# Kernel tuning notes

Measured on AMD Instinct MI355X. Metric: run time of the kernel, lower is better.

Reference implementation:

```python
import jax, jax.numpy as jnp
import numpy as np

N_NODES = 100000
HIDDEN = 128
N_CLASSES = 8


def _sage_conv(x, src, dst, Wl, bl, Wr, num_nodes):
    # PyG SAGEConv (aggr='mean'): out = lin_l(mean_{j in N(i)} x_j) + lin_r(x_i)
    agg = jax.ops.segment_sum(x[src], dst, num_segments=num_nodes)          # [N, H]
    deg = jax.ops.segment_sum(jnp.ones((src.shape[0],), x.dtype), dst,
                              num_segments=num_nodes)                       # [N]
    mean = agg / jnp.maximum(deg, 1.0)[:, None]
    return mean @ Wl + bl + x @ Wr


def setup_inputs() -> dict:
    key = jax.random.key(0)
    ks = jax.random.split(key, 12)
    s = 1.0 / np.sqrt(HIDDEN)
    inp = {
        "node_emb": jax.random.normal(ks[0], (N_NODES, HIDDEN), jnp.float32),
        "Wl0": jax.random.normal(ks[1], (HIDDEN, HIDDEN), jnp.float32) * s,
        "bl0": jnp.zeros((HIDDEN,), jnp.float32),
        "Wr0": jax.random.normal(ks[2], (HIDDEN, HIDDEN), jnp.float32) * s,
        "Wl1": jax.random.normal(ks[3], (HIDDEN, HIDDEN), jnp.float32) * s,
        "bl1": jnp.zeros((HIDDEN,), jnp.float32),
        "Wr1": jax.random.normal(ks[4], (HIDDEN, HIDDEN), jnp.float32) * s,
        "mlp_W1": jax.random.normal(ks[5], (2 * HIDDEN, HIDDEN), jnp.float32) * (1.0 / np.sqrt(2 * HIDDEN)),
        "mlp_b1": jnp.zeros((HIDDEN,), jnp.float32),
        "mlp_W2": jax.random.normal(ks[6], (HIDDEN, N_CLASSES), jnp.float32) * s,
        "mlp_b2": jnp.zeros((N_CLASSES,), jnp.float32),
        "edge_index": jax.random.randint(ks[7], (2, 1600000), 0, N_NODES, jnp.int64),
        "edge_q": jax.random.randint(ks[8], (2, 500000), 0, N_NODES, jnp.int64),
    }
    return inp


def reference(node_emb, Wl0, bl0, Wr0, Wl1, bl1, Wr1,
              mlp_W1, mlp_b1, mlp_W2, mlp_b2, edge_index, edge_q):
    src, dst = edge_index[0], edge_index[1]
    n = node_emb.shape[0]
    # layer 0 + relu (dropout is identity in eval / p=0)
    x = jax.nn.relu(_sage_conv(node_emb, src, dst, Wl0, bl0, Wr0, n))
    # layer 1 + relu
    x = jax.nn.relu(_sage_conv(x, src, dst, Wl1, bl1, Wr1, n))
    # edge classifier: gather endpoint pairs, concat, 2-layer MLP
    qs, qd = edge_q[0], edge_q[1]
    edge_feat = jnp.concatenate([x[qs], x[qd]], axis=-1)   # [Eq, 2H]
    h = jax.nn.relu(edge_feat @ mlp_W1 + mlp_b1)
    logits = h @ mlp_W2 + mlp_b2                            # [Eq, C]
    return logits
```

## Files before the change

kernel.cpp:

```cpp
#include <hip/hip_runtime.h>
#include <hip/hip_bf16.h>
#include <cstdint>
#include <cstddef>

#define HID 128
#define SH 9
#define NODES_PER_BIN 512

typedef __attribute__((ext_vector_type(8))) __bf16 bf16x8;
typedef __attribute__((ext_vector_type(4))) float floatx4;

__device__ __forceinline__ ushort f2bf(float f) {
    uint u = __float_as_uint(f);
    u += 0x7fff + ((u >> 16) & 1);
    return (ushort)(u >> 16);
}
__device__ __forceinline__ float bf2f(uint h) { return __uint_as_float(h << 16); }

__device__ __forceinline__ void async16(const ushort* g, ushort* l) {
    __builtin_amdgcn_global_load_lds(
        (const __attribute__((address_space(1))) uint*)g,
        (__attribute__((address_space(3))) uint*)l, 16, 0, 0);
}


__global__ void k_hist(const int* __restrict__ dst, int E, int* __restrict__ binc) {
    __shared__ int h[256];
    int t = threadIdx.x;
    h[t] = 0;
    __syncthreads();
    for (int e = blockIdx.x * 256 + t; e < E; e += gridDim.x * 256)
        atomicAdd(&h[dst[e] >> SH], 1);
    __syncthreads();
    if (h[t]) atomicAdd(&binc[t], h[t]);
}

__global__ void k_binscan(const int* __restrict__ binc, int* __restrict__ bin_start,
                          int* __restrict__ bin_cursor, int E) {
    __shared__ int s[256];
    int t = threadIdx.x;
    int c = binc[t];
    s[t] = c;
    __syncthreads();
    #pragma unroll
    for (int off = 1; off < 256; off <<= 1) {
        int add = (t >= off) ? s[t - off] : 0;
        __syncthreads();
        s[t] += add;
        __syncthreads();
    }
    int excl = s[t] - c;
    bin_start[t] = excl;
    bin_cursor[t] = excl;
    if (t == 255) bin_start[256] = E;
}

__global__ __launch_bounds__(256) void k_part(
    const int* __restrict__ src, const int* __restrict__ dst, int E,
    int* __restrict__ bin_cursor, uint* __restrict__ ebuf) {
    __shared__ int h[256];
    __shared__ int sc[256];
    __shared__ int rk[256];
    __shared__ int gb[256];
    __shared__ uint2 ro[2048];
    int t = threadIdx.x;
    int base = blockIdx.x * 2048;
    h[t] = 0;
    __syncthreads();
    int dd[8], ss[8];
    bool ok[8];
    #pragma unroll
    for (int k = 0; k < 8; ++k) {
        int e = base + k * 256 + t;
        ok[k] = e < E;
        if (ok[k]) {
            dd[k] = dst[e];
            ss[k] = src[e];
            atomicAdd(&h[dd[k] >> SH], 1);
        }
    }
    __syncthreads();
    sc[t] = h[t];
    __syncthreads();
    #pragma unroll
    for (int off = 1; off < 256; off <<= 1) {
        int add = (t >= off) ? sc[t - off] : 0;
        __syncthreads();
        sc[t] += add;
        __syncthreads();
    }
    rk[t] = sc[t] - h[t];
    {
        int c = h[t];
        if (c > 0) gb[t] = atomicAdd(&bin_cursor[t], c);
    }
    __syncthreads();
    #pragma unroll
    for (int k = 0; k < 8; ++k) {
        if (ok[k]) {
            int bin = dd[k] >> SH;
            int r = atomicAdd(&rk[bin], 1);
            ro[r] = make_uint2((uint)dd[k],
                               ((uint)(dd[k] & (NODES_PER_BIN - 1)) << 23) | (uint)ss[k]);
        }
    }
    __syncthreads();
    int nv = sc[255];
    for (int i = t; i < nv; i += 256) {
        uint2 pr = ro[i];
        int bin = (int)(pr.x >> SH);
        int excl = sc[bin] - h[bin];
        ebuf[gb[bin] + (i - excl)] = pr.y;
    }
}

__global__ __launch_bounds__(256) void k_csr(
    const uint* __restrict__ ebuf, const int* __restrict__ bin_start,
    int* __restrict__ rowptr, int* __restrict__ csr, int N, int E, int NB) {
    __shared__ int cnt[512];
    __shared__ int p[256];
    __shared__ int excl[512];
    int t = threadIdx.x;
    int b = blockIdx.x;
    int d0 = b << SH;
    int ebase = bin_start[b], eend = bin_start[b + 1];
    cnt[t] = 0; cnt[t + 256] = 0;
    __syncthreads();
    for (int e = ebase + t; e < eend; e += 256)
        atomicAdd(&cnt[ebuf[e] >> 23], 1);
    __syncthreads();
    p[t] = cnt[2 * t] + cnt[2 * t + 1];
    __syncthreads();
    #pragma unroll
    for (int off = 1; off < 256; off <<= 1) {
        int add = (t >= off) ? p[t - off] : 0;
        __syncthreads();
        p[t] += add;
        __syncthreads();
    }
    int e0 = (t == 0) ? 0 : p[t - 1];
    excl[2 * t] = e0;
    excl[2 * t + 1] = e0 + cnt[2 * t];
    __syncthreads();
    #pragma unroll
    for (int i = t; i < 512; i += 256) {
        int node = d0 + i;
        if (node < N) rowptr[node] = ebase + excl[i];
    }
    if (b == NB - 1 && t == 0) rowptr[N] = E;
    __syncthreads();
    for (int e = ebase + t; e < eend; e += 256) {
        uint w = ebuf[e];
        int r = atomicAdd(&excl[w >> 23], 1);
        csr[ebase + r] = (int)(w & 0x7FFFFFu);
    }
}


__global__ void k_cvt(const float* __restrict__ in, ushort* __restrict__ out, int n4) {
    int i = blockIdx.x * blockDim.x + threadIdx.x;
    if (i < n4) {
        float4 v = ((const float4*)in)[i];
        ushort4 o;
        o.x = f2bf(v.x); o.y = f2bf(v.y); o.z = f2bf(v.z); o.w = f2bf(v.w);
        ((ushort4*)out)[i] = o;
    }
}

__global__ void k_prepw(const float* __restrict__ Wl0, const float* __restrict__ Wr0,
                        const float* __restrict__ Wl1, const float* __restrict__ Wr1,
                        const float* __restrict__ W1,  const float* __restrict__ W2,
                        ushort* __restrict__ WlrT0, ushort* __restrict__ WlrT1,
                        ushort* __restrict__ W1T,   ushort* __restrict__ W2T) {
    int idx = blockIdx.x * 256 + threadIdx.x;
    if (idx < 32768) {
        int n = idx >> 8, k = idx & 255;
        float v = (k < 128) ? Wl0[k * 128 + n] : Wr0[(k - 128) * 128 + n];
        WlrT0[n * 256 + k] = f2bf(v);
    } else if (idx < 65536) {
        int t = idx - 32768; int n = t >> 8, k = t & 255;
        float v = (k < 128) ? Wl1[k * 128 + n] : Wr1[(k - 128) * 128 + n];
        WlrT1[n * 256 + k] = f2bf(v);
    } else if (idx < 98304) {
        int t = idx - 65536; int n = t >> 8, k = t & 255;
        W1T[n * 256 + k] = f2bf(W1[k * 128 + n]);
    } else if (idx < 100352) {
        int t = idx - 98304; int n = t >> 7, k = t & 127;
        W2T[n * 128 + k] = (n < 8) ? f2bf(W2[k * 8 + n]) : (ushort)0;
    }
}

__global__ __launch_bounds__(256) void k_agg16(const ushort* __restrict__ x,
                                               const int* __restrict__ rowptr,
                                               const int* __restrict__ csr,
                                               ushort* __restrict__ mean, int N) {
    int node = blockIdx.x * 4 + (threadIdx.x >> 6);
    if (node >= N) return;
    int l = threadIdx.x & 63;
    int lh = l & 31, hi = l >> 5;
    int b = rowptr[node], e = rowptr[node + 1];
    const uint2* xv = (const uint2*)x;
    float a0 = 0.f, a1 = 0.f, a2 = 0.f, a3 = 0.f;
    for (int j = b; j < e; j += 4) {
        int r0 = j + hi, r1 = j + 2 + hi;
        if (r0 < e) {
            uint2 v = xv[(size_t)csr[r0] * 32 + lh];
            a0 += bf2f(v.x & 0xffffu); a1 += bf2f(v.x >> 16);
            a2 += bf2f(v.y & 0xffffu); a3 += bf2f(v.y >> 16);
        }
        if (r1 < e) {
            uint2 v = xv[(size_t)csr[r1] * 32 + lh];
            a0 += bf2f(v.x & 0xffffu); a1 += bf2f(v.x >> 16);
            a2 += bf2f(v.y & 0xffffu); a3 += bf2f(v.y >> 16);
        }
    }
    a0 += __shfl_xor(a0, 32);
    a1 += __shfl_xor(a1, 32);
    a2 += __shfl_xor(a2, 32);
    a3 += __shfl_xor(a3, 32);
    if (hi == 0) {
        float inv = 1.f / fmaxf((float)(e - b), 1.f);
        uint2 o;
        o.x = (uint)f2bf(a0 * inv) | ((uint)f2bf(a1 * inv) << 16);
        o.y = (uint)f2bf(a2 * inv) | ((uint)f2bf(a3 * inv) << 16);
        ((uint2*)mean)[(size_t)node * 32 + lh] = o;
    }
}

__global__ __launch_bounds__(256) void k_gemm16(
    const ushort* __restrict__ Alo, const ushort* __restrict__ Ahi,
    const ushort* __restrict__ WT, const float* __restrict__ bias,
    ushort* __restrict__ out, int M) {
    __shared__ ushort As[4096];
    __shared__ ushort Bs[4096];
    int tid = threadIdx.x;
    int l = tid & 63, w = tid >> 6;
    int i0 = blockIdx.x * 128;
    int c0 = w * 64 + l, c1 = c0 + 256;
    int rA0 = c0 >> 2, sA0 = (c0 & 3) * 8;
    int rA1 = c1 >> 2, sA1 = (c1 & 3) * 8;
    int g0 = i0 + rA0; if (g0 >= M) g0 = M - 1;
    int g1 = i0 + rA1; if (g1 >= M) g1 = M - 1;
    int lm = l & 15, lq = l >> 4;

    floatx4 acc[2][8];
    #pragma unroll
    for (int rt = 0; rt < 2; rt++)
        #pragma unroll
        for (int ct = 0; ct < 8; ct++) acc[rt][ct] = (floatx4){0.f, 0.f, 0.f, 0.f};

    for (int kt = 0; kt < 8; ++kt) {
        const ushort* Asrc = (kt < 4) ? Alo : Ahi;
        int kb = (kt & 3) * 32;
        async16(Asrc + (size_t)g0 * 128 + kb + sA0, As + w * 512);
        async16(Asrc + (size_t)g1 * 128 + kb + sA1, As + 2048 + w * 512);
        async16(WT + rA0 * 256 + kt * 32 + sA0, Bs + w * 512);
        async16(WT + rA1 * 256 + kt * 32 + sA1, Bs + 2048 + w * 512);
        __syncthreads();
        bf16x8 a0 = *(const bf16x8*)(As + (w * 32 + lm) * 32 + lq * 8);
        bf16x8 a1 = *(const bf16x8*)(As + (w * 32 + 16 + lm) * 32 + lq * 8);
        #pragma unroll
        for (int ct = 0; ct < 8; ++ct) {
            bf16x8 b = *(const bf16x8*)(Bs + (ct * 16 + lm) * 32 + lq * 8);
            acc[0][ct] = __builtin_amdgcn_mfma_f32_16x16x32_bf16(a0, b, acc[0][ct], 0, 0, 0);
            acc[1][ct] = __builtin_amdgcn_mfma_f32_16x16x32_bf16(a1, b, acc[1][ct], 0, 0, 0);
        }
        __syncthreads();
    }

    float bv[8];
    #pragma unroll
    for (int ct = 0; ct < 8; ++ct) bv[ct] = bias[ct * 16 + lm];
    #pragma unroll
    for (int rt = 0; rt < 2; ++rt)
        #pragma unroll
        for (int ct = 0; ct < 8; ++ct)
            #pragma unroll
            for (int r = 0; r < 4; ++r) {
                int grow = i0 + w * 32 + rt * 16 + lq * 4 + r;
                if (grow < M)
                    out[(size_t)grow * 128 + ct * 16 + lm] =
                        f2bf(fmaxf(acc[rt][ct][r] + bv[ct], 0.f));
            }
}

#define HSTR 136

__global__ __launch_bounds__(256) void k_mlp(
    const ushort* __restrict__ x16, const int* __restrict__ qs, const int* __restrict__ qd,
    const ushort* __restrict__ W1T, const float* __restrict__ b1,
    const ushort* __restrict__ W2T, const float* __restrict__ b2,
    float* __restrict__ out, int Eq) {
    __shared__ union {
        struct { ushort As[4096]; ushort Bs[4096]; } s1;
        struct { ushort Hs[128 * HSTR]; ushort W2s[16 * HSTR]; } s2;
    } sm;
    __shared__ int Ns[256];
    int tid = threadIdx.x;
    int l = tid & 63, w = tid >> 6;
    int lm = l & 15, lq = l >> 4;
    int e0 = blockIdx.x * 128;
    {
        int r = tid & 127;
        int e = e0 + r; if (e >= Eq) e = Eq - 1;
        Ns[tid] = (tid < 128) ? qs[e] : qd[e];
    }
    __syncthreads();

    int c0 = w * 64 + l, c1 = c0 + 256;
    int rA0 = c0 >> 2, sA0 = (c0 & 3) * 8;
    int rA1 = c1 >> 2, sA1 = (c1 & 3) * 8;
    ushort* As = sm.s1.As;
    ushort* Bs = sm.s1.Bs;

    floatx4 acc[2][8];
    #pragma unroll
    for (int rt = 0; rt < 2; rt++)
        #pragma unroll
        for (int ct = 0; ct < 8; ct++) acc[rt][ct] = (floatx4){0.f, 0.f, 0.f, 0.f};

    for (int kt = 0; kt < 8; ++kt) {
        int kb = (kt & 3) * 32;
        const int* Nbase = (kt < 4) ? Ns : (Ns + 128);
        int n0 = Nbase[rA0], n1 = Nbase[rA1];
        async16(x16 + (size_t)n0 * 128 + kb + sA0, As + w * 512);
        async16(x16 + (size_t)n1 * 128 + kb + sA1, As + 2048 + w * 512);
        async16(W1T + rA0 * 256 + kt * 32 + sA0, Bs + w * 512);
        async16(W1T + rA1 * 256 + kt * 32 + sA1, Bs + 2048 + w * 512);
        __syncthreads();
        bf16x8 a0 = *(const bf16x8*)(As + (w * 32 + lm) * 32 + lq * 8);
        bf16x8 a1 = *(const bf16x8*)(As + (w * 32 + 16 + lm) * 32 + lq * 8);
        #pragma unroll
        for (int ct = 0; ct < 8; ++ct) {
            bf16x8 b = *(const bf16x8*)(Bs + (ct * 16 + lm) * 32 + lq * 8);
            acc[0][ct] = __builtin_amdgcn_mfma_f32_16x16x32_bf16(a0, b, acc[0][ct], 0, 0, 0);
            acc[1][ct] = __builtin_amdgcn_mfma_f32_16x16x32_bf16(a1, b, acc[1][ct], 0, 0, 0);
        }
        __syncthreads();
    }

    float b1v[8];
    #pragma unroll
    for (int ct = 0; ct < 8; ++ct) b1v[ct] = b1[ct * 16 + lm];
    #pragma unroll
    for (int rt = 0; rt < 2; ++rt)
        #pragma unroll
        for (int ct = 0; ct < 8; ++ct)
            #pragma unroll
            for (int r = 0; r < 4; ++r) {
                int row = w * 32 + rt * 16 + lq * 4 + r;
                int col = ct * 16 + lm;
                sm.s2.Hs[row * HSTR + col] = f2bf(fmaxf(acc[rt][ct][r] + b1v[ct], 0.f));
            }
    {
        int n = tid >> 4, kc = (tid & 15) * 8;
        #pragma unroll
        for (int j = 0; j < 8; ++j)
            sm.s2.W2s[n * HSTR + kc + j] = W2T[n * 128 + kc + j];
    }
    __syncthreads();

    floatx4 acc2[2];
    acc2[0] = (floatx4){0.f, 0.f, 0.f, 0.f};
    acc2[1] = (floatx4){0.f, 0.f, 0.f, 0.f};
    #pragma unroll
    for (int ks = 0; ks < 4; ++ks) {
        bf16x8 bw = *(const bf16x8*)(sm.s2.W2s + lm * HSTR + ks * 32 + lq * 8);
        bf16x8 h0 = *(const bf16x8*)(sm.s2.Hs + (w * 32 + lm) * HSTR + ks * 32 + lq * 8);
        bf16x8 h1 = *(const bf16x8*)(sm.s2.Hs + (w * 32 + 16 + lm) * HSTR + ks * 32 + lq * 8);
        acc2[0] = __builtin_amdgcn_mfma_f32_16x16x32_bf16(h0, bw, acc2[0], 0, 0, 0);
        acc2[1] = __builtin_amdgcn_mfma_f32_16x16x32_bf16(h1, bw, acc2[1], 0, 0, 0);
    }
    if (lm < 8) {
        float bb = b2[lm];
        #pragma unroll
        for (int rt = 0; rt < 2; ++rt)
            #pragma unroll
            for (int r = 0; r < 4; ++r) {
                int eg = e0 + w * 32 + rt * 16 + lq * 4 + r;
                if (eg < Eq) out[(size_t)eg * 8 + lm] = acc2[rt][r] + bb;
            }
    }
}


extern "C" void kernel_launch(void* const* d_in, const int* in_sizes, int n_in,
                              void* d_out, int out_size, void* d_ws, size_t ws_size,
                              hipStream_t stream) {
    const float* node_emb = (const float*)d_in[0];
    const float* Wl0 = (const float*)d_in[1];
    const float* bl0 = (const float*)d_in[2];
    const float* Wr0 = (const float*)d_in[3];
    const float* Wl1 = (const float*)d_in[4];
    const float* bl1 = (const float*)d_in[5];
    const float* Wr1 = (const float*)d_in[6];
    const float* W1  = (const float*)d_in[7];
    const float* b1  = (const float*)d_in[8];
    const float* W2  = (const float*)d_in[9];
    const float* b2  = (const float*)d_in[10];
    const int* eidx  = (const int*)d_in[11];
    const int* eq    = (const int*)d_in[12];

    int N  = in_sizes[0] / HID;
    int E  = in_sizes[11] / 2;
    int Eq = in_sizes[12] / 2;
    const int* srcp = eidx;
    const int* dstp = eidx + E;
    const int* qs = eq;
    const int* qd = eq + Eq;
    float* outp = (float*)d_out;
    int NB = (N + NODES_PER_BIN - 1) >> SH;

    char* ws = (char*)d_ws;
    size_t off = 0;
    auto take = [&](size_t bytes) -> char* {
        char* p = ws + off;
        off += (bytes + 255) & ~(size_t)255;
        return p;
    };
    int* binc       = (int*)take(256 * 4);
    int* bin_start  = (int*)take(257 * 4);
    int* bin_cursor = (int*)take(256 * 4);
    int* rowptr     = (int*)take((size_t)(N + 1) * 4);
    int* csr        = (int*)take((size_t)E * 4);
    char* meanreg   = take((size_t)N * HID * 2);
    uint* ebuf      = (uint*)meanreg;
    ushort* mean16  = (ushort*)meanreg;
    ushort* x0_16   = (ushort*)take((size_t)N * HID * 2);
    ushort* xa16    = (ushort*)take((size_t)N * HID * 2);
    ushort* xb16    = x0_16;
    ushort* WlrT0   = (ushort*)take(32768 * 2);
    ushort* WlrT1   = (ushort*)take(32768 * 2);
    ushort* W1T     = (ushort*)take(32768 * 2);
    ushort* W2T     = (ushort*)take(2048 * 2);

    hipMemsetAsync(binc, 0, 256 * 4, stream);

    k_hist<<<256, 256, 0, stream>>>(dstp, E, binc);
    k_binscan<<<1, 256, 0, stream>>>(binc, bin_start, bin_cursor, E);
    int pb = (E + 2047) / 2048;
    k_part<<<pb, 256, 0, stream>>>(srcp, dstp, E, bin_cursor, ebuf);
    k_csr<<<NB, 256, 0, stream>>>(ebuf, bin_start, rowptr, csr, N, E, NB);

    int n4 = N * HID / 4;
    const int TB = 256;
    k_cvt<<<(n4 + TB - 1) / TB, TB, 0, stream>>>(node_emb, x0_16, n4);
    k_prepw<<<392, 256, 0, stream>>>(Wl0, Wr0, Wl1, Wr1, W1, W2, WlrT0, WlrT1, W1T, W2T);

    int ab = (N + 3) / 4;
    int mg = (N + 127) / 128;
    k_agg16<<<ab, 256, 0, stream>>>(x0_16, rowptr, csr, mean16, N);
    k_gemm16<<<mg, 256, 0, stream>>>(mean16, x0_16, WlrT0, bl0, xa16, N);
    k_agg16<<<ab, 256, 0, stream>>>(xa16, rowptr, csr, mean16, N);
    k_gemm16<<<mg, 256, 0, stream>>>(mean16, xa16, WlrT1, bl1, xb16, N);

    int eg = (Eq + 127) / 128;
    k_mlp<<<eg, 256, 0, stream>>>(xb16, qs, qd, W1T, b1, W2T, b2, outp, Eq);
}
```

Before: 470.0 us.

## Aggregate over feature-sliced node layout to keep gather working set cache-resident

Node features are also written in a sliced layout (8 slices of 16 features, each stored contiguously across all nodes) by the conversion kernel and the first GEMM epilogue. A new aggregation kernel assigns each block one slice and a chunk of nodes, so each gather reads 32 bytes per neighbor from a 3.2MB slice that can stay in cache. The intent is to improve cache hit rate for the random neighbor gathers. In exchange it adds extra scattered writes and an extra buffer, reads each row's CSR indices eight times, and uses shorter per-edge loads.

```diff
diff --git a/kernel.cpp b/kernel.cpp
--- a/kernel.cpp
+++ b/kernel.cpp
@@ -16,6 +16,9 @@
     return (ushort)(u >> 16);
 }
 __device__ __forceinline__ float bf2f(uint h) { return __uint_as_float(h << 16); }
+__device__ __forceinline__ uint pack2(float a, float b) {
+    return (uint)f2bf(a) | ((uint)f2bf(b) << 16);
+}
 
 __device__ __forceinline__ void async16(const ushort* g, ushort* l) {
     __builtin_amdgcn_global_load_lds(
@@ -157,13 +160,20 @@
 }
 
 
-__global__ void k_cvt(const float* __restrict__ in, ushort* __restrict__ out, int n4) {
+__global__ void k_cvt(const float* __restrict__ in, ushort* __restrict__ out,
+                      uint* __restrict__ XS, int n4, int N) {
     int i = blockIdx.x * blockDim.x + threadIdx.x;
     if (i < n4) {
         float4 v = ((const float4*)in)[i];
-        ushort4 o;
-        o.x = f2bf(v.x); o.y = f2bf(v.y); o.z = f2bf(v.z); o.w = f2bf(v.w);
-        ((ushort4*)out)[i] = o;
+        uint p0 = pack2(v.x, v.y);
+        uint p1 = pack2(v.z, v.w);
+        ((uint2*)out)[i] = make_uint2(p0, p1);
+        int node = i >> 5;
+        int u0 = (i & 31) * 2;
+        int s = u0 >> 3, w0 = u0 & 7;
+        uint* dstp = XS + ((size_t)s * N + node) * 8 + w0;
+        dstp[0] = p0;
+        dstp[1] = p1;
     }
 }
 
@@ -190,47 +200,41 @@
     }
 }
 
-__global__ __launch_bounds__(256) void k_agg16(const ushort* __restrict__ x,
-                                               const int* __restrict__ rowptr,
-                                               const int* __restrict__ csr,
-                                               ushort* __restrict__ mean, int N) {
-    int node = blockIdx.x * 4 + (threadIdx.x >> 6);
-    if (node >= N) return;
-    int l = threadIdx.x & 63;
-    int lh = l & 31, hi = l >> 5;
-    int b = rowptr[node], e = rowptr[node + 1];
-    const uint2* xv = (const uint2*)x;
-    float a0 = 0.f, a1 = 0.f, a2 = 0.f, a3 = 0.f;
-    for (int j = b; j < e; j += 4) {
-        int r0 = j + hi, r1 = j + 2 + hi;
-        if (r0 < e) {
-            uint2 v = xv[(size_t)csr[r0] * 32 + lh];
-            a0 += bf2f(v.x & 0xffffu); a1 += bf2f(v.x >> 16);
-            a2 += bf2f(v.y & 0xffffu); a3 += bf2f(v.y >> 16);
-        }
-        if (r1 < e) {
-            uint2 v = xv[(size_t)csr[r1] * 32 + lh];
-            a0 += bf2f(v.x & 0xffffu); a1 += bf2f(v.x >> 16);
-            a2 += bf2f(v.y & 0xffffu); a3 += bf2f(v.y >> 16);
-        }
-    }
-    a0 += __shfl_xor(a0, 32);
-    a1 += __shfl_xor(a1, 32);
-    a2 += __shfl_xor(a2, 32);
-    a3 += __shfl_xor(a3, 32);
-    if (hi == 0) {
-        float inv = 1.f / fmaxf((float)(e - b), 1.f);
-        uint2 o;
-        o.x = (uint)f2bf(a0 * inv) | ((uint)f2bf(a1 * inv) << 16);
-        o.y = (uint)f2bf(a2 * inv) | ((uint)f2bf(a3 * inv) << 16);
-        ((uint2*)mean)[(size_t)node * 32 + lh] = o;
+__global__ __launch_bounds__(256) void k_aggs(const uint* __restrict__ XS,
+                                              const int* __restrict__ rowptr,
+                                              const int* __restrict__ csr,
+                                              ushort* __restrict__ mean, int N) {
+    int s = blockIdx.x & 7;
+    int chunk = blockIdx.x >> 3;
+    int w = threadIdx.x >> 6, l = threadIdx.x & 63;
+    int g = l >> 3, u = l & 7;
+    const uint* xs = XS + (size_t)s * N * 8;
+    int nodeBase = chunk * 64 + w * 16;
+    for (int i = 0; i < 16; ++i) {
+        int node = nodeBase + i;
+        if (node >= N) break;
+        int b = rowptr[node], e = rowptr[node + 1];
+        float a0 = 0.f, a1 = 0.f;
+        #pragma unroll 2
+        for (int j = b + g; j < e; j += 8) {
+            uint v = xs[(size_t)csr[j] * 8 + u];
+            a0 += bf2f(v & 0xffffu);
+            a1 += bf2f(v >> 16);
+        }
+        a0 += __shfl_xor(a0, 8);  a1 += __shfl_xor(a1, 8);
+        a0 += __shfl_xor(a0, 16); a1 += __shfl_xor(a1, 16);
+        a0 += __shfl_xor(a0, 32); a1 += __shfl_xor(a1, 32);
+        if (l < 8) {
+            float inv = 1.f / fmaxf((float)(e - b), 1.f);
+            ((uint*)mean)[(size_t)node * 64 + s * 8 + u] = pack2(a0 * inv, a1 * inv);
+        }
     }
 }
 
 __global__ __launch_bounds__(256) void k_gemm16(
     const ushort* __restrict__ Alo, const ushort* __restrict__ Ahi,
     const ushort* __restrict__ WT, const float* __restrict__ bias,
-    ushort* __restrict__ out, int M) {
+    ushort* __restrict__ out, uint* __restrict__ xs, int M) {
     __shared__ ushort As[4096];
     __shared__ ushort Bs[4096];
     int tid = threadIdx.x;
@@ -271,6 +275,7 @@
     float bv[8];
     #pragma unroll
     for (int ct = 0; ct < 8; ++ct) bv[ct] = bias[ct * 16 + lm];
+    ushort* XSu = (ushort*)xs;
     #pragma unroll
     for (int rt = 0; rt < 2; ++rt)
         #pragma unroll
@@ -278,9 +283,12 @@
             #pragma unroll
             for (int r = 0; r < 4; ++r) {
                 int grow = i0 + w * 32 + rt * 16 + lq * 4 + r;
-                if (grow < M)
-                    out[(size_t)grow * 128 + ct * 16 + lm] =
-                        f2bf(fmaxf(acc[rt][ct][r] + bv[ct], 0.f));
+                if (grow < M) {
+                    ushort hv = f2bf(fmaxf(acc[rt][ct][r] + bv[ct], 0.f));
+                    out[(size_t)grow * 128 + ct * 16 + lm] = hv;
+                    if (XSu)
+                        XSu[((size_t)ct * M + grow) * 16 + lm] = hv;
+                }
             }
 }
 
@@ -428,6 +436,7 @@
     ushort* mean16  = (ushort*)meanreg;
     ushort* x0_16   = (ushort*)take((size_t)N * HID * 2);
     ushort* xa16    = (ushort*)take((size_t)N * HID * 2);
+    uint* XS        = (uint*)take((size_t)N * HID * 2);
     ushort* xb16    = x0_16;
     ushort* WlrT0   = (ushort*)take(32768 * 2);
     ushort* WlrT1   = (ushort*)take(32768 * 2);
@@ -444,15 +453,15 @@
 
     int n4 = N * HID / 4;
     const int TB = 256;
-    k_cvt<<<(n4 + TB - 1) / TB, TB, 0, stream>>>(node_emb, x0_16, n4);
+    k_cvt<<<(n4 + TB - 1) / TB, TB, 0, stream>>>(node_emb, x0_16, XS, n4, N);
     k_prepw<<<392, 256, 0, stream>>>(Wl0, Wr0, Wl1, Wr1, W1, W2, WlrT0, WlrT1, W1T, W2T);
 
-    int ab = (N + 3) / 4;
+    int ag = 8 * ((N + 63) / 64);
     int mg = (N + 127) / 128;
-    k_agg16<<<ab, 256, 0, stream>>>(x0_16, rowptr, csr, mean16, N);
-    k_gemm16<<<mg, 256, 0, stream>>>(mean16, x0_16, WlrT0, bl0, xa16, N);
-    k_agg16<<<ab, 256, 0, stream>>>(xa16, rowptr, csr, mean16, N);
-    k_gemm16<<<mg, 256, 0, stream>>>(mean16, xa16, WlrT1, bl1, xb16, N);
+    k_aggs<<<ag, 256, 0, stream>>>(XS, rowptr, csr, mean16, N);
+    k_gemm16<<<mg, 256, 0, stream>>>(mean16, x0_16, WlrT0, bl0, xa16, XS, N);
+    k_aggs<<<ag, 256, 0, stream>>>(XS, rowptr, csr, mean16, N);
+    k_gemm16<<<mg, 256, 0, stream>>>(mean16, xa16, WlrT1, bl1, xb16, nullptr, N);
 
     int eg = (Eq + 127) / 128;
     k_mlp<<<eg, 256, 0, stream>>>(xb16, qs, qd, W1T, b1, W2T, b2, outp, Eq);
```

New measurement: 642.9 us. +36.8%, slower.
